# Performance work log

Hardware: AMD Instinct MI355X
Metric: run time of the kernel (lower is better)

The kernel has to match this reference:

```python
import jax, jax.numpy as jnp
import numpy as np

IN_CH_IMG = 256
CHANNELS = 256
NUM_CLASSES = 1
NUM_LAYERS = 4  # NUM_FC=3 -> 4 layers
IN_CH = IN_CH_IMG + 256  # pos-enc adds 256 channels
N_INST = 128
N_PTS = 2048

W_SIZES = [IN_CH * CHANNELS, CHANNELS * CHANNELS, CHANNELS * CHANNELS, CHANNELS * NUM_CLASSES]
B_SIZES = [CHANNELS, CHANNELS, CHANNELS, NUM_CLASSES]
NUM_PARAMS = sum(W_SIZES) + sum(B_SIZES)  # 263169


def setup_inputs() -> dict:
    key = jax.random.key(0)
    k1, k2, k3, k4 = jax.random.split(key, 4)
    return {
        "fine_grained_features": jax.random.normal(k1, (N_INST, IN_CH_IMG, N_PTS), dtype=jnp.float32),
        "point_coords": jax.random.uniform(k2, (N_INST, N_PTS, 2), dtype=jnp.float32),
        "parameters": jax.random.normal(k3, (N_INST, NUM_PARAMS), dtype=jnp.float32) * 0.05,
        "pe_gaussian": jax.random.normal(k4, (2, 128), dtype=jnp.float32),
    }


def _parse_params(params):
    # params: [N, NUM_PARAMS]. Weight blocks first, then bias blocks.
    n = params.shape[0]
    out_dims = [CHANNELS, CHANNELS, CHANNELS, NUM_CLASSES]
    in_dims = [IN_CH, CHANNELS, CHANNELS, CHANNELS]
    weights, biases = [], []
    off = 0
    for l in range(NUM_LAYERS):
        weights.append(params[:, off:off + W_SIZES[l]].reshape(n, out_dims[l], in_dims[l]))
        off += W_SIZES[l]
    for l in range(NUM_LAYERS):
        biases.append(params[:, off:off + B_SIZES[l]].reshape(n, out_dims[l], 1))
        off += B_SIZES[l]
    return weights, biases


def reference(fine_grained_features, point_coords, parameters, pe_gaussian):
    n, _, p = fine_grained_features.shape
    # Positional encoding: [N*P, 2] -> [N*P, 128] -> sin/cos -> [N, 256, P]
    loc = (2.0 * point_coords.reshape(n * p, 2) - 1.0) @ pe_gaussian
    loc = 2.0 * np.pi * loc
    pe = jnp.concatenate([jnp.sin(loc), jnp.cos(loc)], axis=1)  # [N*P, 256]
    pe = pe.reshape(n, p, 256).transpose(0, 2, 1)  # [N, 256, P]
    x = jnp.concatenate([pe, fine_grained_features], axis=1)  # [N, IN_CH, P]

    weights, biases = _parse_params(parameters)
    for i, (w, b) in enumerate(zip(weights, biases)):
        x = jnp.einsum('nck,ndc->ndk', x, w) + b
        if i < NUM_LAYERS - 1:
            x = jax.nn.relu(x)
    return x.reshape(-1, NUM_CLASSES, p)  # [N, 1, P]
```

## Files before the change

kernel.cpp:

```cpp
#include <hip/hip_runtime.h>
#include <hip/hip_fp16.h>


#define NI      128
#define NPTS    2048
#define CH      256
#define NPARAM  263169
#define PT      128
#define NTILES  (NPTS / PT)
#define ROWS    536

#define WOFF0   0
#define WOFF1   131072
#define WOFF2   196608
#define WOFF3   262144
#define BOFF0   262400
#define BOFF1   262656
#define BOFF2   262912
#define BOFF3   263168

#define PI_L0   0
#define PI_L1   131072
#define PI_L2   196608
#define PI_L3   262144
#define WS_PER_INST 262400
#define WS_BYTES ((size_t)NI * WS_PER_INST * 2)

typedef __fp16   h16x2 __attribute__((ext_vector_type(2)));
typedef _Float16 f16x8 __attribute__((ext_vector_type(8)));
typedef float    f32x4 __attribute__((ext_vector_type(4)));

union pack8 { h16x2 h[4]; f16x8 v; };

__global__ __launch_bounds__(256) void iph_prep(
    const float* __restrict__ params, _Float16* __restrict__ wsw)
{
    const int inst = blockIdx.y;
    const int r = blockIdx.x * 256 + threadIdx.x;
    if (r >= 32800) return;
    const float* __restrict__ P = params + (size_t)inst * NPARAM;
    _Float16* __restrict__ W = wsw + (size_t)inst * WS_PER_INST;

    int rl, woff, K, dst;
    if (r < 16384)      { rl = r;         woff = WOFF0; K = 512; dst = PI_L0; }
    else if (r < 24576) { rl = r - 16384; woff = WOFF1; K = 256; dst = PI_L1; }
    else if (r < 32768) { rl = r - 24576; woff = WOFF2; K = 256; dst = PI_L2; }
    else {
        const int e = (r - 32768) * 8;
        f16x8 v;
        #pragma unroll
        for (int j = 0; j < 8; ++j) v[j] = (_Float16)P[WOFF3 + e + j];
        *(f16x8*)&W[PI_L3 + e] = v;
        return;
    }
    const int e    = rl * 8;
    const int lane = rl & 63;
    const int cb   = (rl >> 6) & 15;
    const int ks   = rl >> 10;
    const int co   = (cb >> 1) * 32 + 2 * (lane & 15) + (cb & 1);
    const int k    = ks * 32 + (lane >> 4) * 8;
    const float* __restrict__ src = P + woff + co * K + k;
    f16x8 v;
    #pragma unroll
    for (int j = 0; j < 8; ++j) v[j] = (_Float16)src[j];
    *(f16x8*)&W[dst + e] = v;
}

__device__ __forceinline__ void issue_b2(const _Float16* p, f16x8& r0, f16x8& r1) {
    const unsigned long long a = (unsigned long long)p;
    asm volatile("global_load_dwordx4 %0, %2, off\n\t"
                 "global_load_dwordx4 %1, %2, off offset:1024"
                 : "=&v"(r0), "=&v"(r1)
                 : "v"(a));
}

template<int N>
__device__ __forceinline__ void wait_vm() {
    if constexpr (N >= 8)      asm volatile("s_waitcnt vmcnt(8)" ::: "memory");
    else if constexpr (N == 6) asm volatile("s_waitcnt vmcnt(6)" ::: "memory");
    else if constexpr (N == 4) asm volatile("s_waitcnt vmcnt(4)" ::: "memory");
    else if constexpr (N == 2) asm volatile("s_waitcnt vmcnt(2)" ::: "memory");
    else                       asm volatile("s_waitcnt vmcnt(0)" ::: "memory");
    __builtin_amdgcn_sched_barrier(0);
}

__device__ __forceinline__ void lgkm0_barrier() {
    asm volatile("s_waitcnt lgkmcnt(0)" ::: "memory");
    __builtin_amdgcn_s_barrier();
}

__device__ __forceinline__ void issue_pro(const _Float16* bp, f16x8 (&b0s)[5], f16x8 (&b1s)[5]) {
    #pragma unroll
    for (int i = 0; i < 4; ++i)
        issue_b2(bp + i * 8192, b0s[i], b1s[i]);
}

template<int NKS>
__device__ __forceinline__ void gemm_pipe(
    f32x4 (&acc)[8][2], const _Float16* bp, const _Float16* ap,
    f16x8 (&b0s)[5], f16x8 (&b1s)[5])
{
    #pragma unroll
    for (int ks = 0; ks < NKS; ++ks) {
        f16x8 a[8];
        #pragma unroll
        for (int mt = 0; mt < 8; ++mt)
            a[mt] = *(const f16x8*)(ap + mt * 16 * ROWS + ks * 32);
        if (ks + 4 < NKS)
            issue_b2(bp + (ks + 4) * 8192, b0s[(ks + 4) % 5], b1s[(ks + 4) % 5]);
        const int rem = NKS - 1 - ks;
        if (rem >= 4)      wait_vm<8>();
        else if (rem == 3) wait_vm<6>();
        else if (rem == 2) wait_vm<4>();
        else if (rem == 1) wait_vm<2>();
        else               wait_vm<0>();
        __builtin_amdgcn_s_setprio(1);
        #pragma unroll
        for (int mt = 0; mt < 8; ++mt) {
            acc[mt][0] = __builtin_amdgcn_mfma_f32_16x16x32_f16(a[mt], b0s[ks % 5], acc[mt][0], 0, 0, 0);
            acc[mt][1] = __builtin_amdgcn_mfma_f32_16x16x32_f16(a[mt], b1s[ks % 5], acc[mt][1], 0, 0, 0);
        }
        __builtin_amdgcn_s_setprio(0);
    }
}

template<bool PREPPED>
__global__ __launch_bounds__(512) void iph_main(
    const float* __restrict__ feat,
    const float* __restrict__ coords,
    const float* __restrict__ params,
    const _Float16* __restrict__ wsw,
    const float* __restrict__ peg,
    float* __restrict__ out)
{
    __shared__ _Float16 X[PT * ROWS];
    __shared__ float    partial[8][PT];

    const int bid  = blockIdx.x;
    const int inst = (bid & 7) | ((bid >> 7) << 3);
    const int tile = (bid >> 3) & 15;
    const int p0   = tile * PT;
    const int tid  = threadIdx.x;
    const int lane = tid & 63;
    const int wave = tid >> 6;
    const int l15  = lane & 15;
    const int hi   = lane >> 4;
    const float* __restrict__ P = params + (size_t)inst * NPARAM;
    const _Float16* __restrict__ WI = wsw + (size_t)inst * WS_PER_INST;

    const _Float16* bp0 = WI + PI_L0 + ((wave * 2) * 64 + lane) * 8;
    const _Float16* bp1 = WI + PI_L1 + ((wave * 2) * 64 + lane) * 8;
    const _Float16* bp2 = WI + PI_L2 + ((wave * 2) * 64 + lane) * 8;
    const _Float16* ap  = &X[l15 * ROWS + hi * 8];

    const float2 bb0 = *(const float2*)&P[BOFF0 + wave * 32 + 2 * l15];
    const float2 bb1 = *(const float2*)&P[BOFF1 + wave * 32 + 2 * l15];
    const float2 bb2 = *(const float2*)&P[BOFF2 + wave * 32 + 2 * l15];
    const float2 w3  = *(const float2*)&P[WOFF3 + wave * 32 + 2 * l15];

    f16x8 s0[5], s1[5], t0[5], t1[5], u0[5], u1[5];

    if (PREPPED) issue_pro(bp0, s0, s1);

    {
        const int pt   = tid >> 2;
        const int part = tid & 3;
        const float2 cc = *(const float2*)&coords[((size_t)inst * NPTS + p0 + pt) * 2];
        const float a = 2.f * cc.x - 1.f;
        const float b = 2.f * cc.y - 1.f;
        float sv[32], cv[32];
        #pragma unroll
        for (int j = 0; j < 32; ++j) {
            const int f = part * 32 + j;
            float locr = a * peg[f] + b * peg[128 + f];
            locr -= floorf(locr);
            sv[j] = __builtin_amdgcn_sinf(locr);
            cv[j] = __builtin_amdgcn_cosf(locr);
        }
        _Float16* base = &X[pt * ROWS + part * 32];
        #pragma unroll
        for (int c = 0; c < 4; ++c) {
            pack8 ps, pc;
            #pragma unroll
            for (int q = 0; q < 4; ++q) {
                ps.h[q] = __builtin_amdgcn_cvt_pkrtz(sv[c*8 + 2*q], sv[c*8 + 2*q + 1]);
                pc.h[q] = __builtin_amdgcn_cvt_pkrtz(cv[c*8 + 2*q], cv[c*8 + 2*q + 1]);
            }
            *(f16x8*)(base + c * 8)       = ps.v;
            *(f16x8*)(base + 128 + c * 8) = pc.v;
        }
    }
    {
        const int p  = tid & 127;
        const int cg = tid >> 7;
        const float* fbase = feat + (size_t)inst * CH * NPTS + (size_t)(cg * 64) * NPTS + p0 + p;
        #pragma unroll
        for (int s = 0; s < 8; ++s) {
            float w8[8];
            #pragma unroll
            for (int j = 0; j < 8; ++j)
                w8[j] = fbase[(size_t)(s * 8 + j) * NPTS];
            pack8 pk;
            #pragma unroll
            for (int q = 0; q < 4; ++q)
                pk.h[q] = __builtin_amdgcn_cvt_pkrtz(w8[2*q], w8[2*q + 1]);
            *(f16x8*)&X[p * ROWS + 256 + cg * 64 + s * 8] = pk.v;
        }
    }
    lgkm0_barrier();

    auto write_epilogue = [&](f32x4 (&acc)[8][2], const float2 bb) {
        #pragma unroll
        for (int mt = 0; mt < 8; ++mt) {
            #pragma unroll
            for (int r = 0; r < 4; ++r) {
                const float v0 = fmaxf(acc[mt][0][r] + bb.x, 0.f);
                const float v1 = fmaxf(acc[mt][1][r] + bb.y, 0.f);
                const h16x2 e = __builtin_amdgcn_cvt_pkrtz(v0, v1);
                const int pt = mt * 16 + hi * 4 + r;
                *(h16x2*)&X[pt * ROWS + wave * 32 + 2 * l15] = e;
            }
        }
    };

    auto gemm_simple = [&](f32x4 (&acc)[8][2], const float* pw, const int K) {
        for (int ks = 0; ks < (K >> 5); ++ks) {
            f16x8 bfrag[2];
            #pragma unroll
            for (int nt = 0; nt < 2; ++nt) {
                const int co = wave * 32 + 2 * l15 + nt;
                const float* wp = pw + (size_t)co * K + ks * 32 + hi * 8;
                float w8[8];
                __builtin_memcpy(w8, wp, 32);
                f16x8 bb;
                #pragma unroll
                for (int j = 0; j < 8; ++j) bb[j] = (_Float16)w8[j];
                bfrag[nt] = bb;
            }
            #pragma unroll
            for (int mt = 0; mt < 8; ++mt) {
                f16x8 af = *(const f16x8*)&X[(mt * 16 + l15) * ROWS + ks * 32 + hi * 8];
                acc[mt][0] = __builtin_amdgcn_mfma_f32_16x16x32_f16(af, bfrag[0], acc[mt][0], 0, 0, 0);
                acc[mt][1] = __builtin_amdgcn_mfma_f32_16x16x32_f16(af, bfrag[1], acc[mt][1], 0, 0, 0);
            }
        }
    };

    {
        f32x4 acc[8][2];
        #pragma unroll
        for (int mt = 0; mt < 8; ++mt)
            #pragma unroll
            for (int nt = 0; nt < 2; ++nt)
                acc[mt][nt] = (f32x4){0.f, 0.f, 0.f, 0.f};
        if (PREPPED) gemm_pipe<16>(acc, bp0, ap, s0, s1);
        else         gemm_simple(acc, P + WOFF0, 512);
        if (PREPPED) issue_pro(bp1, t0, t1);
        __builtin_amdgcn_s_barrier();
        write_epilogue(acc, bb0);
        lgkm0_barrier();
    }
    {
        f32x4 acc[8][2];
        #pragma unroll
        for (int mt = 0; mt < 8; ++mt)
            #pragma unroll
            for (int nt = 0; nt < 2; ++nt)
                acc[mt][nt] = (f32x4){0.f, 0.f, 0.f, 0.f};
        if (PREPPED) gemm_pipe<8>(acc, bp1, ap, t0, t1);
        else         gemm_simple(acc, P + WOFF1, 256);
        if (PREPPED) issue_pro(bp2, u0, u1);
        __builtin_amdgcn_s_barrier();
        write_epilogue(acc, bb1);
        lgkm0_barrier();
    }
    {
        f32x4 acc[8][2];
        #pragma unroll
        for (int mt = 0; mt < 8; ++mt)
            #pragma unroll
            for (int nt = 0; nt < 2; ++nt)
                acc[mt][nt] = (f32x4){0.f, 0.f, 0.f, 0.f};
        if (PREPPED) gemm_pipe<8>(acc, bp2, ap, u0, u1);
        else         gemm_simple(acc, P + WOFF2, 256);
        #pragma unroll
        for (int mt = 0; mt < 8; ++mt) {
            #pragma unroll
            for (int r = 0; r < 4; ++r) {
                const float v0 = fmaxf(acc[mt][0][r] + bb2.x, 0.f);
                const float v1 = fmaxf(acc[mt][1][r] + bb2.y, 0.f);
                float s = v0 * w3.x + v1 * w3.y;
                s += __shfl_xor(s, 1);
                s += __shfl_xor(s, 2);
                s += __shfl_xor(s, 4);
                s += __shfl_xor(s, 8);
                if (l15 == 0)
                    partial[wave][mt * 16 + hi * 4 + r] = s;
            }
        }
        lgkm0_barrier();
        if (tid < PT) {
            float s = P[BOFF3];
            #pragma unroll
            for (int w = 0; w < 8; ++w) s += partial[w][tid];
            out[(size_t)inst * NPTS + p0 + tid] = s;
        }
    }
}

extern "C" void kernel_launch(void* const* d_in, const int* in_sizes, int n_in,
                              void* d_out, int out_size, void* d_ws, size_t ws_size,
                              hipStream_t stream) {
    (void)in_sizes; (void)n_in; (void)out_size;
    const float* feat   = (const float*)d_in[0];
    const float* coords = (const float*)d_in[1];
    const float* params = (const float*)d_in[2];
    const float* peg    = (const float*)d_in[3];
    float* out = (float*)d_out;

    dim3 grid(NI * NTILES);
    dim3 block(512);

    if (ws_size >= WS_BYTES) {
        _Float16* wsw = (_Float16*)d_ws;
        iph_prep<<<dim3(129, 128), dim3(256), 0, stream>>>(params, wsw);
        iph_main<true><<<grid, block, 0, stream>>>(feat, coords, params, wsw, peg, out);
    } else {
        iph_main<false><<<grid, block, 0, stream>>>(feat, coords, params,
                                                    (const _Float16*)d_ws, peg, out);
    }
}
```

Baseline: 246.7 us.

## Halve point tile and block size, give each wave a 4x4 MFMA tile

The point tile shrinks from 128 to 64 and the block from 512 to 256 threads, so each wave now covers 64 output channels by 64 points with a 4x4 grid of MFMA accumulators instead of 8x2. Weight prefetching changes to groups of four dwordx4 loads with a three-stage ring in place of pairs with a four-stage ring. The smaller LDS footprint and block size are meant to let more blocks run per CU and improve per-wave register reuse. In exchange, each weight matrix is fetched by twice as many blocks, doubling weight traffic from cache, and the prefetch depth is shallower.

```diff
diff --git a/kernel.cpp b/kernel.cpp
--- a/kernel.cpp
+++ b/kernel.cpp
@@ -6,7 +6,7 @@
 #define NPTS    2048
 #define CH      256
 #define NPARAM  263169
-#define PT      128
+#define PT      64
 #define NTILES  (NPTS / PT)
 #define ROWS    536
 
@@ -66,20 +66,22 @@
     *(f16x8*)&W[dst + e] = v;
 }
 
-__device__ __forceinline__ void issue_b2(const _Float16* p, f16x8& r0, f16x8& r1) {
+__device__ __forceinline__ void issue_b4(const _Float16* p,
+                                         f16x8& r0, f16x8& r1, f16x8& r2, f16x8& r3) {
     const unsigned long long a = (unsigned long long)p;
-    asm volatile("global_load_dwordx4 %0, %2, off\n\t"
-                 "global_load_dwordx4 %1, %2, off offset:1024"
-                 : "=&v"(r0), "=&v"(r1)
+    asm volatile("global_load_dwordx4 %0, %4, off\n\t"
+                 "global_load_dwordx4 %1, %4, off offset:1024\n\t"
+                 "global_load_dwordx4 %2, %4, off offset:2048\n\t"
+                 "global_load_dwordx4 %3, %4, off offset:3072"
+                 : "=&v"(r0), "=&v"(r1), "=&v"(r2), "=&v"(r3)
                  : "v"(a));
 }
 
 template<int N>
 __device__ __forceinline__ void wait_vm() {
-    if constexpr (N >= 8)      asm volatile("s_waitcnt vmcnt(8)" ::: "memory");
-    else if constexpr (N == 6) asm volatile("s_waitcnt vmcnt(6)" ::: "memory");
+    if constexpr (N >= 12)     asm volatile("s_waitcnt vmcnt(12)" ::: "memory");
+    else if constexpr (N == 8) asm volatile("s_waitcnt vmcnt(8)" ::: "memory");
     else if constexpr (N == 4) asm volatile("s_waitcnt vmcnt(4)" ::: "memory");
-    else if constexpr (N == 2) asm volatile("s_waitcnt vmcnt(2)" ::: "memory");
     else                       asm volatile("s_waitcnt vmcnt(0)" ::: "memory");
     __builtin_amdgcn_sched_barrier(0);
 }
@@ -89,43 +91,46 @@
     __builtin_amdgcn_s_barrier();
 }
 
-__device__ __forceinline__ void issue_pro(const _Float16* bp, f16x8 (&b0s)[5], f16x8 (&b1s)[5]) {
+__device__ __forceinline__ void issue_pro(const _Float16* bp, f16x8 (&q)[4][4]) {
     #pragma unroll
-    for (int i = 0; i < 4; ++i)
-        issue_b2(bp + i * 8192, b0s[i], b1s[i]);
+    for (int i = 0; i < 3; ++i)
+        issue_b4(bp + i * 8192, q[i][0], q[i][1], q[i][2], q[i][3]);
 }
 
 template<int NKS>
 __device__ __forceinline__ void gemm_pipe(
-    f32x4 (&acc)[8][2], const _Float16* bp, const _Float16* ap,
-    f16x8 (&b0s)[5], f16x8 (&b1s)[5])
+    f32x4 (&acc)[4][4], const _Float16* bp, const _Float16* ap, f16x8 (&q)[4][4])
 {
     #pragma unroll
     for (int ks = 0; ks < NKS; ++ks) {
-        f16x8 a[8];
-        #pragma unroll
-        for (int mt = 0; mt < 8; ++mt)
+        f16x8 a[4];
+        #pragma unroll
+        for (int mt = 0; mt < 4; ++mt)
             a[mt] = *(const f16x8*)(ap + mt * 16 * ROWS + ks * 32);
-        if (ks + 4 < NKS)
-            issue_b2(bp + (ks + 4) * 8192, b0s[(ks + 4) % 5], b1s[(ks + 4) % 5]);
+        if (ks + 3 < NKS) {
+            const int s = (ks + 3) & 3;
+            issue_b4(bp + (ks + 3) * 8192, q[s][0], q[s][1], q[s][2], q[s][3]);
+        }
         const int rem = NKS - 1 - ks;
-        if (rem >= 4)      wait_vm<8>();
-        else if (rem == 3) wait_vm<6>();
-        else if (rem == 2) wait_vm<4>();
-        else if (rem == 1) wait_vm<2>();
+        if (rem >= 3)      wait_vm<12>();
+        else if (rem == 2) wait_vm<8>();
+        else if (rem == 1) wait_vm<4>();
         else               wait_vm<0>();
+        const int c = ks & 3;
         __builtin_amdgcn_s_setprio(1);
         #pragma unroll
-        for (int mt = 0; mt < 8; ++mt) {
-            acc[mt][0] = __builtin_amdgcn_mfma_f32_16x16x32_f16(a[mt], b0s[ks % 5], acc[mt][0], 0, 0, 0);
-            acc[mt][1] = __builtin_amdgcn_mfma_f32_16x16x32_f16(a[mt], b1s[ks % 5], acc[mt][1], 0, 0, 0);
+        for (int mt = 0; mt < 4; ++mt) {
+            acc[mt][0] = __builtin_amdgcn_mfma_f32_16x16x32_f16(a[mt], q[c][0], acc[mt][0], 0, 0, 0);
+            acc[mt][1] = __builtin_amdgcn_mfma_f32_16x16x32_f16(a[mt], q[c][1], acc[mt][1], 0, 0, 0);
+            acc[mt][2] = __builtin_amdgcn_mfma_f32_16x16x32_f16(a[mt], q[c][2], acc[mt][2], 0, 0, 0);
+            acc[mt][3] = __builtin_amdgcn_mfma_f32_16x16x32_f16(a[mt], q[c][3], acc[mt][3], 0, 0, 0);
         }
         __builtin_amdgcn_s_setprio(0);
     }
 }
 
 template<bool PREPPED>
-__global__ __launch_bounds__(512) void iph_main(
+__global__ __launch_bounds__(256) void iph_main(
     const float* __restrict__ feat,
     const float* __restrict__ coords,
     const float* __restrict__ params,
@@ -134,11 +139,11 @@
     float* __restrict__ out)
 {
     __shared__ _Float16 X[PT * ROWS];
-    __shared__ float    partial[8][PT];
+    __shared__ float    partial[4][PT];
 
     const int bid  = blockIdx.x;
-    const int inst = (bid & 7) | ((bid >> 7) << 3);
-    const int tile = (bid >> 3) & 15;
+    const int inst = (bid & 7) | ((bid >> 8) << 3);
+    const int tile = (bid >> 3) & 31;
     const int p0   = tile * PT;
     const int tid  = threadIdx.x;
     const int lane = tid & 63;
@@ -148,19 +153,23 @@
     const float* __restrict__ P = params + (size_t)inst * NPARAM;
     const _Float16* __restrict__ WI = wsw + (size_t)inst * WS_PER_INST;
 
-    const _Float16* bp0 = WI + PI_L0 + ((wave * 2) * 64 + lane) * 8;
-    const _Float16* bp1 = WI + PI_L1 + ((wave * 2) * 64 + lane) * 8;
-    const _Float16* bp2 = WI + PI_L2 + ((wave * 2) * 64 + lane) * 8;
+    const _Float16* bp0 = WI + PI_L0 + ((wave * 4) * 64 + lane) * 8;
+    const _Float16* bp1 = WI + PI_L1 + ((wave * 4) * 64 + lane) * 8;
+    const _Float16* bp2 = WI + PI_L2 + ((wave * 4) * 64 + lane) * 8;
     const _Float16* ap  = &X[l15 * ROWS + hi * 8];
 
-    const float2 bb0 = *(const float2*)&P[BOFF0 + wave * 32 + 2 * l15];
-    const float2 bb1 = *(const float2*)&P[BOFF1 + wave * 32 + 2 * l15];
-    const float2 bb2 = *(const float2*)&P[BOFF2 + wave * 32 + 2 * l15];
-    const float2 w3  = *(const float2*)&P[WOFF3 + wave * 32 + 2 * l15];
-
-    f16x8 s0[5], s1[5], t0[5], t1[5], u0[5], u1[5];
-
-    if (PREPPED) issue_pro(bp0, s0, s1);
+    const float2 b0l = *(const float2*)&P[BOFF0 + wave * 64 + 2 * l15];
+    const float2 b0h = *(const float2*)&P[BOFF0 + wave * 64 + 32 + 2 * l15];
+    const float2 b1l = *(const float2*)&P[BOFF1 + wave * 64 + 2 * l15];
+    const float2 b1h = *(const float2*)&P[BOFF1 + wave * 64 + 32 + 2 * l15];
+    const float2 b2l = *(const float2*)&P[BOFF2 + wave * 64 + 2 * l15];
+    const float2 b2h = *(const float2*)&P[BOFF2 + wave * 64 + 32 + 2 * l15];
+    const float2 w3l = *(const float2*)&P[WOFF3 + wave * 64 + 2 * l15];
+    const float2 w3h = *(const float2*)&P[WOFF3 + wave * 64 + 32 + 2 * l15];
+
+    f16x8 qa[4][4], qb[4][4], qc[4][4];
+
+    if (PREPPED) issue_pro(bp0, qa);
 
     {
         const int pt   = tid >> 2;
@@ -191,8 +200,8 @@
         }
     }
     {
-        const int p  = tid & 127;
-        const int cg = tid >> 7;
+        const int p  = tid & 63;
+        const int cg = tid >> 6;
         const float* fbase = feat + (size_t)inst * CH * NPTS + (size_t)(cg * 64) * NPTS + p0 + p;
         #pragma unroll
         for (int s = 0; s < 8; ++s) {
@@ -209,26 +218,29 @@
     }
     lgkm0_barrier();
 
-    auto write_epilogue = [&](f32x4 (&acc)[8][2], const float2 bb) {
-        #pragma unroll
-        for (int mt = 0; mt < 8; ++mt) {
+    auto write_epilogue = [&](f32x4 (&acc)[4][4], const float2 bl, const float2 bh) {
+        #pragma unroll
+        for (int mt = 0; mt < 4; ++mt) {
             #pragma unroll
             for (int r = 0; r < 4; ++r) {
-                const float v0 = fmaxf(acc[mt][0][r] + bb.x, 0.f);
-                const float v1 = fmaxf(acc[mt][1][r] + bb.y, 0.f);
-                const h16x2 e = __builtin_amdgcn_cvt_pkrtz(v0, v1);
                 const int pt = mt * 16 + hi * 4 + r;
-                *(h16x2*)&X[pt * ROWS + wave * 32 + 2 * l15] = e;
+                const float v0 = fmaxf(acc[mt][0][r] + bl.x, 0.f);
+                const float v1 = fmaxf(acc[mt][1][r] + bl.y, 0.f);
+                const float v2 = fmaxf(acc[mt][2][r] + bh.x, 0.f);
+                const float v3 = fmaxf(acc[mt][3][r] + bh.y, 0.f);
+                *(h16x2*)&X[pt * ROWS + wave * 64 + 2 * l15]      = __builtin_amdgcn_cvt_pkrtz(v0, v1);
+                *(h16x2*)&X[pt * ROWS + wave * 64 + 32 + 2 * l15] = __builtin_amdgcn_cvt_pkrtz(v2, v3);
             }
         }
     };
 
-    auto gemm_simple = [&](f32x4 (&acc)[8][2], const float* pw, const int K) {
+    auto gemm_simple = [&](f32x4 (&acc)[4][4], const float* pw, const int K) {
         for (int ks = 0; ks < (K >> 5); ++ks) {
-            f16x8 bfrag[2];
-            #pragma unroll
-            for (int nt = 0; nt < 2; ++nt) {
-                const int co = wave * 32 + 2 * l15 + nt;
+            f16x8 bfrag[4];
+            #pragma unroll
+            for (int nt = 0; nt < 4; ++nt) {
+                const int cb = wave * 4 + nt;
+                const int co = (cb >> 1) * 32 + 2 * l15 + (cb & 1);
                 const float* wp = pw + (size_t)co * K + ks * 32 + hi * 8;
                 float w8[8];
                 __builtin_memcpy(w8, wp, 32);
@@ -238,58 +250,61 @@
                 bfrag[nt] = bb;
             }
             #pragma unroll
-            for (int mt = 0; mt < 8; ++mt) {
+            for (int mt = 0; mt < 4; ++mt) {
                 f16x8 af = *(const f16x8*)&X[(mt * 16 + l15) * ROWS + ks * 32 + hi * 8];
-                acc[mt][0] = __builtin_amdgcn_mfma_f32_16x16x32_f16(af, bfrag[0], acc[mt][0], 0, 0, 0);
-                acc[mt][1] = __builtin_amdgcn_mfma_f32_16x16x32_f16(af, bfrag[1], acc[mt][1], 0, 0, 0);
+                #pragma unroll
+                for (int nt = 0; nt < 4; ++nt)
+                    acc[mt][nt] = __builtin_amdgcn_mfma_f32_16x16x32_f16(af, bfrag[nt], acc[mt][nt], 0, 0, 0);
             }
         }
     };
 
     {
-        f32x4 acc[8][2];
-        #pragma unroll
-        for (int mt = 0; mt < 8; ++mt)
-            #pragma unroll
-            for (int nt = 0; nt < 2; ++nt)
+        f32x4 acc[4][4];
+        #pragma unroll
+        for (int mt = 0; mt < 4; ++mt)
+            #pragma unroll
+            for (int nt = 0; nt < 4; ++nt)
                 acc[mt][nt] = (f32x4){0.f, 0.f, 0.f, 0.f};
-        if (PREPPED) gemm_pipe<16>(acc, bp0, ap, s0, s1);
+        if (PREPPED) gemm_pipe<16>(acc, bp0, ap, qa);
         else         gemm_simple(acc, P + WOFF0, 512);
-        if (PREPPED) issue_pro(bp1, t0, t1);
+        if (PREPPED) issue_pro(bp1, qb);
         __builtin_amdgcn_s_barrier();
-        write_epilogue(acc, bb0);
+        write_epilogue(acc, b0l, b0h);
         lgkm0_barrier();
     }
     {
-        f32x4 acc[8][2];
-        #pragma unroll
-        for (int mt = 0; mt < 8; ++mt)
-            #pragma unroll
-            for (int nt = 0; nt < 2; ++nt)
+        f32x4 acc[4][4];
+        #pragma unroll
+        for (int mt = 0; mt < 4; ++mt)
+            #pragma unroll
+            for (int nt = 0; nt < 4; ++nt)
                 acc[mt][nt] = (f32x4){0.f, 0.f, 0.f, 0.f};
-        if (PREPPED) gemm_pipe<8>(acc, bp1, ap, t0, t1);
+        if (PREPPED) gemm_pipe<8>(acc, bp1, ap, qb);
         else         gemm_simple(acc, P + WOFF1, 256);
-        if (PREPPED) issue_pro(bp2, u0, u1);
+        if (PREPPED) issue_pro(bp2, qc);
         __builtin_amdgcn_s_barrier();
-        write_epilogue(acc, bb1);
+        write_epilogue(acc, b1l, b1h);
         lgkm0_barrier();
     }
     {
-        f32x4 acc[8][2];
-        #pragma unroll
-        for (int mt = 0; mt < 8; ++mt)
-            #pragma unroll
-            for (int nt = 0; nt < 2; ++nt)
+        f32x4 acc[4][4];
+        #pragma unroll
+        for (int mt = 0; mt < 4; ++mt)
+            #pragma unroll
+            for (int nt = 0; nt < 4; ++nt)
                 acc[mt][nt] = (f32x4){0.f, 0.f, 0.f, 0.f};
-        if (PREPPED) gemm_pipe<8>(acc, bp2, ap, u0, u1);
+        if (PREPPED) gemm_pipe<8>(acc, bp2, ap, qc);
         else         gemm_simple(acc, P + WOFF2, 256);
         #pragma unroll
-        for (int mt = 0; mt < 8; ++mt) {
+        for (int mt = 0; mt < 4; ++mt) {
             #pragma unroll
             for (int r = 0; r < 4; ++r) {
-                const float v0 = fmaxf(acc[mt][0][r] + bb2.x, 0.f);
-                const float v1 = fmaxf(acc[mt][1][r] + bb2.y, 0.f);
-                float s = v0 * w3.x + v1 * w3.y;
+                const float v0 = fmaxf(acc[mt][0][r] + b2l.x, 0.f);
+                const float v1 = fmaxf(acc[mt][1][r] + b2l.y, 0.f);
+                const float v2 = fmaxf(acc[mt][2][r] + b2h.x, 0.f);
+                const float v3 = fmaxf(acc[mt][3][r] + b2h.y, 0.f);
+                float s = v0 * w3l.x + v1 * w3l.y + v2 * w3h.x + v3 * w3h.y;
                 s += __shfl_xor(s, 1);
                 s += __shfl_xor(s, 2);
                 s += __shfl_xor(s, 4);
@@ -302,7 +317,7 @@
         if (tid < PT) {
             float s = P[BOFF3];
             #pragma unroll
-            for (int w = 0; w < 8; ++w) s += partial[w][tid];
+            for (int w = 0; w < 4; ++w) s += partial[w][tid];
             out[(size_t)inst * NPTS + p0 + tid] = s;
         }
     }
@@ -319,7 +334,7 @@
     float* out = (float*)d_out;
 
     dim3 grid(NI * NTILES);
-    dim3 block(512);
+    dim3 block(256);
 
     if (ws_size >= WS_BYTES) {
         _Float16* wsw = (_Float16*)d_ws;
```

Result: slower. 286.0 us (+15.9%).
